# Performance work log

Hardware: AMD Instinct MI355X
Metric: run time of the kernel (lower is better)

Reference implementation:

```python
import jax, jax.numpy as jnp
import numpy as np

NUM_EMBED = 204
HEAD_DIM = 64
B, T = 4, 4096


def setup_inputs() -> dict:
    key = jax.random.key(0)
    kx, kq, kk, kv = jax.random.split(key, 4)
    x = jax.random.normal(kx, (B, T, NUM_EMBED), dtype=jnp.float32)
    s = 1.0 / np.sqrt(NUM_EMBED)
    Wq = jax.random.normal(kq, (NUM_EMBED, HEAD_DIM), dtype=jnp.float32) * s
    Wk = jax.random.normal(kk, (NUM_EMBED, HEAD_DIM), dtype=jnp.float32) * s
    Wv = jax.random.normal(kv, (NUM_EMBED, HEAD_DIM), dtype=jnp.float32) * s
    return {"x": x, "Wq": Wq, "Wk": Wk, "Wv": Wv, "mask": True}


def reference(x, Wq, Wk, Wv, mask):
    # Single-head causal attention. d_k = x.shape[-1] (as in the source, which
    # scales by sqrt of the INPUT embed dim, not head_dim).
    Bn, Tn, d_k = x.shape
    q = x @ Wq  # [B,T,H]
    k = x @ Wk  # [B,T,H]
    v = x @ Wv  # [B,T,H]
    scale = 1.0 / jnp.sqrt(jnp.asarray(d_k, dtype=x.dtype))
    scores = jnp.einsum("bqh,bkh->bqk", q, k) * scale  # [B,T,T]
    if mask:
        causal = jnp.tril(jnp.ones((Tn, Tn), dtype=bool))  # allow j <= i
        scores = jnp.where(causal, scores, jnp.finfo(scores.dtype).min)
    attn = jax.nn.softmax(scores, axis=-1)
    out = jnp.einsum("bqk,bkh->bqh", attn, v)  # [B,T,H]
    # dropout is identity in eval mode
    return out
```

## Files before the change

### kernel.cpp

```cpp
#include <hip/hip_runtime.h>

#define TSEQ   4096
#define NB     4
#define EMB    204
#define HD     64
#define WK     224
#define XSTR   232
#define KSTR   72
#define VSTR   136
#define PSTR   68
#define BIG_NEG (-3.0e38f)

typedef __attribute__((ext_vector_type(8))) short bf16x8;
typedef __attribute__((ext_vector_type(4))) float f32x4;

__device__ __forceinline__ short f2bf(float f) {
    unsigned u = __float_as_uint(f);
    return (short)((u + 0x7fffu + ((u >> 16) & 1u)) >> 16);
}
__device__ __forceinline__ float bf2f(short h) {
    return __uint_as_float(((unsigned)(unsigned short)h) << 16);
}

__global__ __launch_bounds__(256) void prep_zero_kernel(
    const float* __restrict__ Wq,
    const float* __restrict__ Wk,
    const float* __restrict__ Wv,
    short* __restrict__ Wt,
    float* __restrict__ zacc)
{
    int f = blockIdx.x * 256 + threadIdx.x;
    if (f < 3 * HD * WK) {
        int e   = f % WK;
        int h   = (f / WK) % HD;
        int mat = f / (WK * HD);
        const float* W = (mat == 0) ? Wq : (mat == 1) ? Wk : Wv;
        float v = (e < EMB) ? W[e * HD + h] : 0.f;
        Wt[f] = f2bf(v);
    }
    for (int c = blockIdx.x * 256 + threadIdx.x; c < 266240; c += 256 * 256)
        *(float4*)(zacc + c * 4) = make_float4(0.f, 0.f, 0.f, 0.f);
}

__global__ __launch_bounds__(192) void qkv_mfma_kernel(
    const float* __restrict__ x,
    const short* __restrict__ Wt,
    short* __restrict__ qg,
    short* __restrict__ kg,
    short* __restrict__ vtg)
{
    __shared__ __align__(16) short xs[16 * XSTR];

    const int t    = threadIdx.x;
    const int lane = t & 63;
    const int w    = t >> 6;
    const int l15  = lane & 15;
    const int quad = lane >> 4;
    const long long rowb = (long long)blockIdx.x * 16;

    for (int c = t; c < 816; c += 192) {
        int r = c / 51, c4 = c % 51;
        float4 xv = *(const float4*)(x + (rowb + r) * EMB + c4 * 4);
        unsigned p0 = (unsigned)(unsigned short)f2bf(xv.x)
                    | ((unsigned)(unsigned short)f2bf(xv.y) << 16);
        unsigned p1 = (unsigned)(unsigned short)f2bf(xv.z)
                    | ((unsigned)(unsigned short)f2bf(xv.w) << 16);
        uint2 pk; pk.x = p0; pk.y = p1;
        *(uint2*)(&xs[r * XSTR + c4 * 4]) = pk;
    }
    for (int c = t; c < 16 * 28; c += 192) {
        int r = c / 28, cc = c % 28;
        xs[r * XSTR + EMB + cc] = 0;
    }
    __syncthreads();

    f32x4 acc[4];
#pragma unroll
    for (int nt = 0; nt < 4; ++nt) acc[nt] = (f32x4){0.f, 0.f, 0.f, 0.f};

    const short* Wb = Wt + (size_t)w * HD * WK;
#pragma unroll
    for (int ks = 0; ks < 7; ++ks) {
        bf16x8 af = *(const bf16x8*)(&xs[l15 * XSTR + ks * 32 + quad * 8]);
#pragma unroll
        for (int nt = 0; nt < 4; ++nt) {
            bf16x8 bfr = *(const bf16x8*)(Wb + (size_t)(nt * 16 + l15) * WK
                                          + ks * 32 + quad * 8);
            acc[nt] = __builtin_amdgcn_mfma_f32_16x16x32_bf16(af, bfr, acc[nt], 0, 0, 0);
        }
    }

    const float scale = 0.07001400420f;
    if (w == 0) {
#pragma unroll
        for (int r = 0; r < 4; ++r) {
            long long grow = rowb + quad * 4 + r;
#pragma unroll
            for (int nt = 0; nt < 4; ++nt)
                qg[grow * HD + nt * 16 + l15] = f2bf(acc[nt][r] * scale);
        }
    } else if (w == 1) {
#pragma unroll
        for (int r = 0; r < 4; ++r) {
            long long grow = rowb + quad * 4 + r;
#pragma unroll
            for (int nt = 0; nt < 4; ++nt)
                kg[grow * HD + nt * 16 + l15] = f2bf(acc[nt][r]);
        }
    } else {
#pragma unroll
        for (int r = 0; r < 4; ++r) {
            long long grow = rowb + quad * 4 + r;
            int bb = (int)(grow >> 12);
            int tt = (int)(grow & 4095);
#pragma unroll
            for (int nt = 0; nt < 4; ++nt)
                vtg[((long long)bb * HD + nt * 16 + l15) * TSEQ + tt] = f2bf(acc[nt][r]);
        }
    }
}

__global__ __launch_bounds__(256) void flash_mfma_kernel(
    const short* __restrict__ qg,
    const short* __restrict__ kg,
    const short* __restrict__ vtg,
    float* __restrict__ outacc,
    float* __restrict__ lacc)
{
    __shared__ __align__(16) short Ks[128 * KSTR];
    __shared__ __align__(16) short Vt[HD * VSTR];
    __shared__ __align__(16) short Ps[4 * 16 * PSTR];

    const int t    = threadIdx.x;
    const int lane = t & 63;
    const int w    = t >> 6;
    const int pair = w & 1;
    const int par  = w >> 1;
    const int l15  = lane & 15;
    const int quad = lane >> 4;

    const int b = blockIdx.y;
    const int p = 319 - (int)blockIdx.x;

    int a, idx, s;
    if (p < 32)       { a = p >> 2;                idx = p & 3;           s = 1; }
    else if (p < 96)  { a = 8 + ((p - 32) >> 3);   idx = (p - 32) & 7;    s = 2; }
    else if (p < 192) { a = 16 + (p - 96) / 12;    idx = (p - 96) % 12;   s = 3; }
    else              { a = 24 + ((p - 192) >> 4); idx = (p - 192) & 15;  s = 4; }
    const int qt    = 4 * a + idx / s;
    const int split = idx % s;
    const int ntiles = a + 1;
    const int chunk  = (ntiles + s - 1) / s;
    const int kt0    = split * chunk;
    const int kt1    = min(ntiles, kt0 + chunk);

    const int qbase = qt * 32;
    const long long rowb = (long long)b * TSEQ;

    bf16x8 aq[2];
#pragma unroll
    for (int ss = 0; ss < 2; ++ss)
        aq[ss] = *(const bf16x8*)(qg + (rowb + qbase + pair * 16 + l15) * HD
                                  + ss * 32 + quad * 8);

    f32x4 Oacc[4];
#pragma unroll
    for (int nt = 0; nt < 4; ++nt) Oacc[nt] = (f32x4){0.f, 0.f, 0.f, 0.f};
    float lsum[4] = {0.f, 0.f, 0.f, 0.f};

    short* pw = &Ps[w * 16 * PSTR];

    for (int kt = kt0; kt < kt1; ++kt) {
        const int k0 = kt * 128;
        const bool masked = (kt == ntiles - 1);
        __syncthreads();

#pragma unroll
        for (int i = 0; i < 4; ++i) {
            int c = t + i * 256;
            int r = c >> 3, c8 = (c & 7) * 8;
            *(int4*)(&Ks[r * KSTR + c8]) =
                *(const int4*)(kg + (rowb + k0 + r) * HD + c8);
        }
#pragma unroll
        for (int i = 0; i < 4; ++i) {
            int c = t + i * 256;
            int r = c >> 4, c8 = (c & 15) * 8;
            *(int4*)(&Vt[r * VSTR + c8]) =
                *(const int4*)(vtg + ((long long)b * HD + r) * TSEQ + k0 + c8);
        }
        __syncthreads();

        f32x4 S[4];
#pragma unroll
        for (int nt = 0; nt < 4; ++nt) S[nt] = (f32x4){0.f, 0.f, 0.f, 0.f};
#pragma unroll
        for (int ss = 0; ss < 2; ++ss) {
#pragma unroll
            for (int nt = 0; nt < 4; ++nt) {
                bf16x8 bk = *(const bf16x8*)(&Ks[(par * 64 + nt * 16 + l15) * KSTR
                                                 + ss * 32 + quad * 8]);
                S[nt] = __builtin_amdgcn_mfma_f32_16x16x32_bf16(aq[ss], bk, S[nt], 0, 0, 0);
            }
        }

        if (!masked) {
#pragma unroll
            for (int r = 0; r < 4; ++r) {
#pragma unroll
                for (int nt = 0; nt < 4; ++nt) {
                    float pv = __expf(S[nt][r]);
                    short h = f2bf(pv);
                    pw[(quad * 4 + r) * PSTR + nt * 16 + l15] = h;
                    lsum[r] += bf2f(h);
                }
            }
        } else {
#pragma unroll
            for (int r = 0; r < 4; ++r) {
                const int irow = qbase + pair * 16 + quad * 4 + r;
#pragma unroll
                for (int nt = 0; nt < 4; ++nt) {
                    int j = k0 + par * 64 + nt * 16 + l15;
                    float pv = (j <= irow) ? __expf(S[nt][r]) : 0.f;
                    short h = f2bf(pv);
                    pw[(quad * 4 + r) * PSTR + nt * 16 + l15] = h;
                    lsum[r] += bf2f(h);
                }
            }
        }

#pragma unroll
        for (int ss = 0; ss < 2; ++ss) {
            bf16x8 pa = *(const bf16x8*)(&pw[l15 * PSTR + ss * 32 + quad * 8]);
#pragma unroll
            for (int nt = 0; nt < 4; ++nt) {
                bf16x8 vb = *(const bf16x8*)(&Vt[(nt * 16 + l15) * VSTR
                                                 + par * 64 + ss * 32 + quad * 8]);
                Oacc[nt] = __builtin_amdgcn_mfma_f32_16x16x32_bf16(pa, vb, Oacc[nt], 0, 0, 0);
            }
        }
    }

#pragma unroll
    for (int r = 0; r < 4; ++r) {
#pragma unroll
        for (int off = 1; off < 16; off <<= 1)
            lsum[r] += __shfl_xor(lsum[r], off, 64);
    }

    float* oa = outacc + (rowb + qbase + pair * 16) * HD;
#pragma unroll
    for (int r = 0; r < 4; ++r) {
        int row = quad * 4 + r;
#pragma unroll
        for (int nt = 0; nt < 4; ++nt)
            atomicAdd(&oa[row * HD + nt * 16 + l15], Oacc[nt][r]);
        if (l15 == 0)
            atomicAdd(&lacc[rowb + qbase + pair * 16 + row], lsum[r]);
    }
}

__global__ __launch_bounds__(256) void finalize_kernel(
    const float* __restrict__ outacc,
    const float* __restrict__ lacc,
    float* __restrict__ out)
{
    int row = blockIdx.x * 16 + (threadIdx.x >> 4);
    int c4  = (threadIdx.x & 15) * 4;
    float inv = 1.0f / lacc[row];
    float4 v = *(const float4*)(outacc + (size_t)row * HD + c4);
    v.x *= inv; v.y *= inv; v.z *= inv; v.w *= inv;
    *(float4*)(out + (size_t)row * HD + c4) = v;
}

extern "C" void kernel_launch(void* const* d_in, const int* in_sizes, int n_in,
                              void* d_out, int out_size, void* d_ws, size_t ws_size,
                              hipStream_t stream)
{
    const float* x  = (const float*)d_in[0];
    const float* Wq = (const float*)d_in[1];
    const float* Wk = (const float*)d_in[2];
    const float* Wv = (const float*)d_in[3];

    const size_t nrows = (size_t)NB * TSEQ;
    short* qg  = (short*)d_ws;
    short* kg  = qg + nrows * HD;
    short* vtg = kg + nrows * HD;
    short* Wt  = vtg + nrows * HD;
    float* outacc = (float*)(Wt + 3 * HD * WK);
    float* lacc   = outacc + nrows * HD;
    float* outp = (float*)d_out;

    prep_zero_kernel<<<dim3(256), dim3(256), 0, stream>>>(Wq, Wk, Wv, Wt, outacc);
    qkv_mfma_kernel<<<dim3(1024), dim3(192), 0, stream>>>(x, Wt, qg, kg, vtg);
    flash_mfma_kernel<<<dim3(320, NB), dim3(256), 0, stream>>>(qg, kg, vtg, outacc, lacc);
    finalize_kernel<<<dim3(1024), dim3(256), 0, stream>>>(outacc, lacc, outp);
}
```

Measured before the change: 123.8 us.

## Fuse weight prep into QKV kernel, prefetch K/V tiles, compute row sums via MFMA

Merges the weight-transpose and zeroing kernel into the QKV projection kernel. Each block now stages all three bf16 weight matrices in LDS and computes 64 rows of Q, K and V, then writes V^T through an LDS transpose so the global stores are coalesced. In the flash kernel, the next K/V tile is prefetched into registers while the current tile is computed. Softmax row sums are now produced by an MFMA against a ones vector instead of scalar adds and shuffles, and the P stride is padded. The cost is more LDS and registers per block, and each block redundantly reloads and converts the weights.

```diff
diff --git a/kernel.cpp b/kernel.cpp
--- a/kernel.cpp
+++ b/kernel.cpp
@@ -6,9 +6,10 @@
 #define HD     64
 #define WK     224
 #define XSTR   232
+#define WSTR   232
 #define KSTR   72
 #define VSTR   136
-#define PSTR   68
+#define PSTR   72
 #define BIG_NEG (-3.0e38f)
 
 typedef __attribute__((ext_vector_type(8))) short bf16x8;
@@ -18,47 +19,50 @@
     unsigned u = __float_as_uint(f);
     return (short)((u + 0x7fffu + ((u >> 16) & 1u)) >> 16);
 }
-__device__ __forceinline__ float bf2f(short h) {
-    return __uint_as_float(((unsigned)(unsigned short)h) << 16);
-}
-
-__global__ __launch_bounds__(256) void prep_zero_kernel(
+
+__global__ __launch_bounds__(256) void qkv_fused_kernel(
+    const float* __restrict__ x,
     const float* __restrict__ Wq,
     const float* __restrict__ Wk,
     const float* __restrict__ Wv,
-    short* __restrict__ Wt,
-    float* __restrict__ zacc)
-{
-    int f = blockIdx.x * 256 + threadIdx.x;
-    if (f < 3 * HD * WK) {
-        int e   = f % WK;
-        int h   = (f / WK) % HD;
-        int mat = f / (WK * HD);
-        const float* W = (mat == 0) ? Wq : (mat == 1) ? Wk : Wv;
-        float v = (e < EMB) ? W[e * HD + h] : 0.f;
-        Wt[f] = f2bf(v);
-    }
-    for (int c = blockIdx.x * 256 + threadIdx.x; c < 266240; c += 256 * 256)
-        *(float4*)(zacc + c * 4) = make_float4(0.f, 0.f, 0.f, 0.f);
-}
-
-__global__ __launch_bounds__(192) void qkv_mfma_kernel(
-    const float* __restrict__ x,
-    const short* __restrict__ Wt,
     short* __restrict__ qg,
     short* __restrict__ kg,
-    short* __restrict__ vtg)
+    short* __restrict__ vtg,
+    float* __restrict__ outacc,
+    float* __restrict__ lacc)
 {
-    __shared__ __align__(16) short xs[16 * XSTR];
+    __shared__ __align__(16) short xs[64 * XSTR];
+    __shared__ __align__(16) short wl[3 * HD * WSTR];
 
     const int t    = threadIdx.x;
     const int lane = t & 63;
     const int w    = t >> 6;
     const int l15  = lane & 15;
     const int quad = lane >> 4;
-    const long long rowb = (long long)blockIdx.x * 16;
-
-    for (int c = t; c < 816; c += 192) {
+    const long long rowb = (long long)blockIdx.x * 64;
+
+    {
+        float4 z = make_float4(0.f, 0.f, 0.f, 0.f);
+#pragma unroll
+        for (int i = 0; i < 4; ++i)
+            *(float4*)(outacc + rowb * HD + (size_t)(t + i * 256) * 4) = z;
+        if (t < 64) lacc[rowb + t] = 0.f;
+    }
+
+    {
+        const int h = t & 63;
+        const int g = t >> 6;
+#pragma unroll
+        for (int m = 0; m < 3; ++m) {
+            const float* W = (m == 0) ? Wq : (m == 1) ? Wk : Wv;
+            for (int e = g; e < WK; e += 4) {
+                float v = (e < EMB) ? W[e * HD + h] : 0.f;
+                wl[((size_t)m * HD + h) * WSTR + e] = f2bf(v);
+            }
+        }
+    }
+
+    for (int c = t; c < 3264; c += 256) {
         int r = c / 51, c4 = c % 51;
         float4 xv = *(const float4*)(x + (rowb + r) * EMB + c4 * 4);
         unsigned p0 = (unsigned)(unsigned short)f2bf(xv.x)
@@ -68,54 +72,62 @@
         uint2 pk; pk.x = p0; pk.y = p1;
         *(uint2*)(&xs[r * XSTR + c4 * 4]) = pk;
     }
-    for (int c = t; c < 16 * 28; c += 192) {
+    for (int c = t; c < 64 * 28; c += 256) {
         int r = c / 28, cc = c % 28;
         xs[r * XSTR + EMB + cc] = 0;
     }
     __syncthreads();
 
-    f32x4 acc[4];
-#pragma unroll
-    for (int nt = 0; nt < 4; ++nt) acc[nt] = (f32x4){0.f, 0.f, 0.f, 0.f};
-
-    const short* Wb = Wt + (size_t)w * HD * WK;
+    f32x4 acc[3][4];
+#pragma unroll
+    for (int m = 0; m < 3; ++m)
+#pragma unroll
+        for (int nt = 0; nt < 4; ++nt) acc[m][nt] = (f32x4){0.f, 0.f, 0.f, 0.f};
+
 #pragma unroll
     for (int ks = 0; ks < 7; ++ks) {
-        bf16x8 af = *(const bf16x8*)(&xs[l15 * XSTR + ks * 32 + quad * 8]);
+        bf16x8 af = *(const bf16x8*)(&xs[(w * 16 + l15) * XSTR + ks * 32 + quad * 8]);
+#pragma unroll
+        for (int m = 0; m < 3; ++m) {
+#pragma unroll
+            for (int nt = 0; nt < 4; ++nt) {
+                bf16x8 bfr = *(const bf16x8*)(&wl[((size_t)m * HD + nt * 16 + l15) * WSTR
+                                                  + ks * 32 + quad * 8]);
+                acc[m][nt] = __builtin_amdgcn_mfma_f32_16x16x32_bf16(af, bfr, acc[m][nt], 0, 0, 0);
+            }
+        }
+    }
+
+    const float scale = 0.07001400420f;
+#pragma unroll
+    for (int r = 0; r < 4; ++r) {
+        long long grow = rowb + w * 16 + quad * 4 + r;
 #pragma unroll
         for (int nt = 0; nt < 4; ++nt) {
-            bf16x8 bfr = *(const bf16x8*)(Wb + (size_t)(nt * 16 + l15) * WK
-                                          + ks * 32 + quad * 8);
-            acc[nt] = __builtin_amdgcn_mfma_f32_16x16x32_bf16(af, bfr, acc[nt], 0, 0, 0);
-        }
-    }
-
-    const float scale = 0.07001400420f;
-    if (w == 0) {
-#pragma unroll
-        for (int r = 0; r < 4; ++r) {
-            long long grow = rowb + quad * 4 + r;
-#pragma unroll
-            for (int nt = 0; nt < 4; ++nt)
-                qg[grow * HD + nt * 16 + l15] = f2bf(acc[nt][r] * scale);
-        }
-    } else if (w == 1) {
-#pragma unroll
-        for (int r = 0; r < 4; ++r) {
-            long long grow = rowb + quad * 4 + r;
-#pragma unroll
-            for (int nt = 0; nt < 4; ++nt)
-                kg[grow * HD + nt * 16 + l15] = f2bf(acc[nt][r]);
-        }
-    } else {
-#pragma unroll
-        for (int r = 0; r < 4; ++r) {
-            long long grow = rowb + quad * 4 + r;
-            int bb = (int)(grow >> 12);
-            int tt = (int)(grow & 4095);
-#pragma unroll
-            for (int nt = 0; nt < 4; ++nt)
-                vtg[((long long)bb * HD + nt * 16 + l15) * TSEQ + tt] = f2bf(acc[nt][r]);
+            qg[grow * HD + nt * 16 + l15] = f2bf(acc[0][nt][r] * scale);
+            kg[grow * HD + nt * 16 + l15] = f2bf(acc[1][nt][r]);
+        }
+    }
+
+    __syncthreads();
+    short* vts = xs;
+#pragma unroll
+    for (int r = 0; r < 4; ++r) {
+        int tt = w * 16 + quad * 4 + r;
+#pragma unroll
+        for (int nt = 0; nt < 4; ++nt)
+            vts[(nt * 16 + l15) * 72 + tt] = f2bf(acc[2][nt][r]);
+    }
+    __syncthreads();
+    {
+        int bb  = (int)(rowb >> 12);
+        int tt0 = (int)(rowb & 4095);
+#pragma unroll
+        for (int i = 0; i < 2; ++i) {
+            int h = (t >> 3) + i * 32;
+            int c = t & 7;
+            *(int4*)(vtg + ((long long)bb * HD + h) * TSEQ + tt0 + c * 8) =
+                *(const int4*)(&vts[h * 72 + c * 8]);
         }
     }
 }
@@ -147,8 +159,8 @@
     else if (p < 96)  { a = 8 + ((p - 32) >> 3);   idx = (p - 32) & 7;    s = 2; }
     else if (p < 192) { a = 16 + (p - 96) / 12;    idx = (p - 96) % 12;   s = 3; }
     else              { a = 24 + ((p - 192) >> 4); idx = (p - 192) & 15;  s = 4; }
-    const int qt    = 4 * a + idx / s;
-    const int split = idx % s;
+    const int qt     = 4 * a + idx / s;
+    const int split  = idx % s;
     const int ntiles = a + 1;
     const int chunk  = (ntiles + s - 1) / s;
     const int kt0    = split * chunk;
@@ -163,33 +175,55 @@
         aq[ss] = *(const bf16x8*)(qg + (rowb + qbase + pair * 16 + l15) * HD
                                   + ss * 32 + quad * 8);
 
+    bf16x8 ones;
+#pragma unroll
+    for (int j = 0; j < 8; ++j) ones[j] = (short)0x3F80;
+
     f32x4 Oacc[4];
 #pragma unroll
     for (int nt = 0; nt < 4; ++nt) Oacc[nt] = (f32x4){0.f, 0.f, 0.f, 0.f};
-    float lsum[4] = {0.f, 0.f, 0.f, 0.f};
+    f32x4 Lac = (f32x4){0.f, 0.f, 0.f, 0.f};
 
     short* pw = &Ps[w * 16 * PSTR];
 
+    int4 kr[4], vr[4];
+#define LOAD_UNIT(KT)                                                        \
+    {                                                                        \
+        const int _k0 = (KT) * 128;                                          \
+        _Pragma("unroll")                                                    \
+        for (int i = 0; i < 4; ++i) {                                        \
+            int c = t + i * 256;                                             \
+            kr[i] = *(const int4*)(kg + (rowb + _k0 + (c >> 3)) * HD         \
+                                   + (c & 7) * 8);                           \
+        }                                                                    \
+        _Pragma("unroll")                                                    \
+        for (int i = 0; i < 4; ++i) {                                        \
+            int c = t + i * 256;                                             \
+            vr[i] = *(const int4*)(vtg + ((long long)b * HD + (c >> 4)) * TSEQ \
+                                   + _k0 + (c & 15) * 8);                    \
+        }                                                                    \
+    }
+
+    LOAD_UNIT(kt0);
+
     for (int kt = kt0; kt < kt1; ++kt) {
+        const bool masked = (kt == ntiles - 1);
         const int k0 = kt * 128;
-        const bool masked = (kt == ntiles - 1);
         __syncthreads();
 
 #pragma unroll
         for (int i = 0; i < 4; ++i) {
             int c = t + i * 256;
-            int r = c >> 3, c8 = (c & 7) * 8;
-            *(int4*)(&Ks[r * KSTR + c8]) =
-                *(const int4*)(kg + (rowb + k0 + r) * HD + c8);
+            *(int4*)(&Ks[(c >> 3) * KSTR + (c & 7) * 8]) = kr[i];
         }
 #pragma unroll
         for (int i = 0; i < 4; ++i) {
             int c = t + i * 256;
-            int r = c >> 4, c8 = (c & 15) * 8;
-            *(int4*)(&Vt[r * VSTR + c8]) =
-                *(const int4*)(vtg + ((long long)b * HD + r) * TSEQ + k0 + c8);
+            *(int4*)(&Vt[(c >> 4) * VSTR + (c & 15) * 8]) = vr[i];
         }
         __syncthreads();
+
+        if (kt + 1 < kt1) LOAD_UNIT(kt + 1);
 
         f32x4 S[4];
 #pragma unroll
@@ -206,15 +240,10 @@
 
         if (!masked) {
 #pragma unroll
-            for (int r = 0; r < 4; ++r) {
-#pragma unroll
-                for (int nt = 0; nt < 4; ++nt) {
-                    float pv = __expf(S[nt][r]);
-                    short h = f2bf(pv);
-                    pw[(quad * 4 + r) * PSTR + nt * 16 + l15] = h;
-                    lsum[r] += bf2f(h);
-                }
-            }
+            for (int r = 0; r < 4; ++r)
+#pragma unroll
+                for (int nt = 0; nt < 4; ++nt)
+                    pw[(quad * 4 + r) * PSTR + nt * 16 + l15] = f2bf(__expf(S[nt][r]));
         } else {
 #pragma unroll
             for (int r = 0; r < 4; ++r) {
@@ -223,9 +252,7 @@
                 for (int nt = 0; nt < 4; ++nt) {
                     int j = k0 + par * 64 + nt * 16 + l15;
                     float pv = (j <= irow) ? __expf(S[nt][r]) : 0.f;
-                    short h = f2bf(pv);
-                    pw[(quad * 4 + r) * PSTR + nt * 16 + l15] = h;
-                    lsum[r] += bf2f(h);
+                    pw[(quad * 4 + r) * PSTR + nt * 16 + l15] = f2bf(pv);
                 }
             }
         }
@@ -233,6 +260,7 @@
 #pragma unroll
         for (int ss = 0; ss < 2; ++ss) {
             bf16x8 pa = *(const bf16x8*)(&pw[l15 * PSTR + ss * 32 + quad * 8]);
+            Lac = __builtin_amdgcn_mfma_f32_16x16x32_bf16(pa, ones, Lac, 0, 0, 0);
 #pragma unroll
             for (int nt = 0; nt < 4; ++nt) {
                 bf16x8 vb = *(const bf16x8*)(&Vt[(nt * 16 + l15) * VSTR
@@ -241,13 +269,7 @@
             }
         }
     }
-
-#pragma unroll
-    for (int r = 0; r < 4; ++r) {
-#pragma unroll
-        for (int off = 1; off < 16; off <<= 1)
-            lsum[r] += __shfl_xor(lsum[r], off, 64);
-    }
+#undef LOAD_UNIT
 
     float* oa = outacc + (rowb + qbase + pair * 16) * HD;
 #pragma unroll
@@ -257,7 +279,7 @@
         for (int nt = 0; nt < 4; ++nt)
             atomicAdd(&oa[row * HD + nt * 16 + l15], Oacc[nt][r]);
         if (l15 == 0)
-            atomicAdd(&lacc[rowb + qbase + pair * 16 + row], lsum[r]);
+            atomicAdd(&lacc[rowb + qbase + pair * 16 + row], Lac[r]);
     }
 }
 
@@ -287,13 +309,13 @@
     short* qg  = (short*)d_ws;
     short* kg  = qg + nrows * HD;
     short* vtg = kg + nrows * HD;
-    short* Wt  = vtg + nrows * HD;
-    float* outacc = (float*)(Wt + 3 * HD * WK);
+    float* outacc = (float*)(vtg + nrows * HD);
     float* lacc   = outacc + nrows * HD;
     float* outp = (float*)d_out;
 
-    prep_zero_kernel<<<dim3(256), dim3(256), 0, stream>>>(Wq, Wk, Wv, Wt, outacc);
-    qkv_mfma_kernel<<<dim3(1024), dim3(192), 0, stream>>>(x, Wt, qg, kg, vtg);
-    flash_mfma_kernel<<<dim3(320, NB), dim3(256), 0, stream>>>(qg, kg, vtg, outacc, lacc);
+    qkv_fused_kernel<<<dim3(256), dim3(256), 0, stream>>>(
+        x, Wq, Wk, Wv, qg, kg, vtg, outacc, lacc);
+    flash_mfma_kernel<<<dim3(320, NB), dim3(256), 0, stream>>>(
+        qg, kg, vtg, outacc, lacc);
     finalize_kernel<<<dim3(1024), dim3(256), 0, stream>>>(outacc, lacc, outp);
 }
```

Result: slower. 209.7 us (+69.4%).

## Restructure attention as K-block-stationary work units with register-resident K/V

Applied to the files above, without the earlier changes.

Replaces the query-tile flash kernel with a flattened work list of (batch, key block, query 16-row tile) units split evenly across 2048 waves. Each wave keeps a 128-key K and V block in registers, reloading only when the key block changes, and for each query tile computes scores, exp, and the partial output. Every unit then atomically adds its partial output into the accumulator. Row sums come from an MFMA against a ones vector instead of shuffles, and the next Q tile is prefetched. This removes shared-memory K/V staging and block syncs and balances the causal work, at the cost of far more global atomics and heavy register pressure.

```diff
diff --git a/kernel.cpp b/kernel.cpp
--- a/kernel.cpp
+++ b/kernel.cpp
@@ -6,10 +6,7 @@
 #define HD     64
 #define WK     224
 #define XSTR   232
-#define KSTR   72
-#define VSTR   136
-#define PSTR   68
-#define BIG_NEG (-3.0e38f)
+#define PSTR   136
 
 typedef __attribute__((ext_vector_type(8))) short bf16x8;
 typedef __attribute__((ext_vector_type(4))) float f32x4;
@@ -17,9 +14,6 @@
 __device__ __forceinline__ short f2bf(float f) {
     unsigned u = __float_as_uint(f);
     return (short)((u + 0x7fffu + ((u >> 16) & 1u)) >> 16);
-}
-__device__ __forceinline__ float bf2f(short h) {
-    return __uint_as_float(((unsigned)(unsigned short)h) << 16);
 }
 
 __global__ __launch_bounds__(256) void prep_zero_kernel(
@@ -120,144 +114,134 @@
     }
 }
 
-__global__ __launch_bounds__(256) void flash_mfma_kernel(
+__global__ __launch_bounds__(256, 2) void flash_kreg_kernel(
     const short* __restrict__ qg,
     const short* __restrict__ kg,
     const short* __restrict__ vtg,
     float* __restrict__ outacc,
     float* __restrict__ lacc)
 {
-    __shared__ __align__(16) short Ks[128 * KSTR];
-    __shared__ __align__(16) short Vt[HD * VSTR];
     __shared__ __align__(16) short Ps[4 * 16 * PSTR];
 
     const int t    = threadIdx.x;
     const int lane = t & 63;
     const int w    = t >> 6;
-    const int pair = w & 1;
-    const int par  = w >> 1;
     const int l15  = lane & 15;
     const int quad = lane >> 4;
 
-    const int b = blockIdx.y;
-    const int p = 319 - (int)blockIdx.x;
-
-    int a, idx, s;
-    if (p < 32)       { a = p >> 2;                idx = p & 3;           s = 1; }
-    else if (p < 96)  { a = 8 + ((p - 32) >> 3);   idx = (p - 32) & 7;    s = 2; }
-    else if (p < 192) { a = 16 + (p - 96) / 12;    idx = (p - 96) % 12;   s = 3; }
-    else              { a = 24 + ((p - 192) >> 4); idx = (p - 192) & 15;  s = 4; }
-    const int qt    = 4 * a + idx / s;
-    const int split = idx % s;
-    const int ntiles = a + 1;
-    const int chunk  = (ntiles + s - 1) / s;
-    const int kt0    = split * chunk;
-    const int kt1    = min(ntiles, kt0 + chunk);
-
-    const int qbase = qt * 32;
-    const long long rowb = (long long)b * TSEQ;
-
-    bf16x8 aq[2];
-#pragma unroll
-    for (int ss = 0; ss < 2; ++ss)
-        aq[ss] = *(const bf16x8*)(qg + (rowb + qbase + pair * 16 + l15) * HD
-                                  + ss * 32 + quad * 8);
-
-    f32x4 Oacc[4];
-#pragma unroll
-    for (int nt = 0; nt < 4; ++nt) Oacc[nt] = (f32x4){0.f, 0.f, 0.f, 0.f};
-    float lsum[4] = {0.f, 0.f, 0.f, 0.f};
+    const int gw = (int)blockIdx.x * 4 + w;
+    int       u  = (int)(((long long)gw * 16896) >> 11);
+    const int u1 = (int)(((long long)(gw + 1) * 16896) >> 11);
 
     short* pw = &Ps[w * 16 * PSTR];
 
-    for (int kt = kt0; kt < kt1; ++kt) {
-        const int k0 = kt * 128;
-        const bool masked = (kt == ntiles - 1);
-        __syncthreads();
-
-#pragma unroll
-        for (int i = 0; i < 4; ++i) {
-            int c = t + i * 256;
-            int r = c >> 3, c8 = (c & 7) * 8;
-            *(int4*)(&Ks[r * KSTR + c8]) =
-                *(const int4*)(kg + (rowb + k0 + r) * HD + c8);
-        }
-#pragma unroll
-        for (int i = 0; i < 4; ++i) {
-            int c = t + i * 256;
-            int r = c >> 4, c8 = (c & 15) * 8;
-            *(int4*)(&Vt[r * VSTR + c8]) =
-                *(const int4*)(vtg + ((long long)b * HD + r) * TSEQ + k0 + c8);
-        }
-        __syncthreads();
-
-        f32x4 S[4];
-#pragma unroll
-        for (int nt = 0; nt < 4; ++nt) S[nt] = (f32x4){0.f, 0.f, 0.f, 0.f};
-#pragma unroll
-        for (int ss = 0; ss < 2; ++ss) {
-#pragma unroll
-            for (int nt = 0; nt < 4; ++nt) {
-                bf16x8 bk = *(const bf16x8*)(&Ks[(par * 64 + nt * 16 + l15) * KSTR
-                                                 + ss * 32 + quad * 8]);
-                S[nt] = __builtin_amdgcn_mfma_f32_16x16x32_bf16(aq[ss], bk, S[nt], 0, 0, 0);
+    int b  = u / 4224;
+    int r0 = u - b * 4224;
+    int kb = 0;
+    while (r0 >= 256 - 8 * kb) { r0 -= 256 - 8 * kb; ++kb; }
+    int qi = r0;
+
+    bf16x8 ones;
+#pragma unroll
+    for (int j = 0; j < 8; ++j) ones[j] = (short)0x3F80;
+
+    bf16x8 bk[8][2];
+    bf16x8 vb[4][4];
+    long long rowb = (long long)b * TSEQ;
+    int curkb = -1, curb = -1;
+
+    bf16x8 aq[2], aqn[2];
+    {
+        const short* qr = qg + (rowb + kb * 128 + qi * 16 + l15) * HD + quad * 8;
+        aq[0] = *(const bf16x8*)(qr);
+        aq[1] = *(const bf16x8*)(qr + 32);
+    }
+
+    for (; u < u1; ++u) {
+        if (kb != curkb || b != curb) {
+            curkb = kb; curb = b;
+            const int j0r = kb * 128;
+#pragma unroll
+            for (int nt = 0; nt < 8; ++nt) {
+                const short* kr = kg + (rowb + j0r + nt * 16 + l15) * HD + quad * 8;
+                bk[nt][0] = *(const bf16x8*)(kr);
+                bk[nt][1] = *(const bf16x8*)(kr + 32);
             }
+#pragma unroll
+            for (int ss = 0; ss < 4; ++ss)
+#pragma unroll
+                for (int nt = 0; nt < 4; ++nt)
+                    vb[ss][nt] = *(const bf16x8*)(vtg + ((long long)b * HD + nt * 16 + l15) * TSEQ
+                                                  + j0r + ss * 32 + quad * 8);
+        }
+        const int j0 = kb * 128;
+        const int q0 = j0 + qi * 16;
+        const bool masked = (qi < 8);
+
+        f32x4 S[8];
+#pragma unroll
+        for (int nt = 0; nt < 8; ++nt) S[nt] = (f32x4){0.f, 0.f, 0.f, 0.f};
+#pragma unroll
+        for (int ss = 0; ss < 2; ++ss)
+#pragma unroll
+            for (int nt = 0; nt < 8; ++nt)
+                S[nt] = __builtin_amdgcn_mfma_f32_16x16x32_bf16(aq[ss], bk[nt][ss], S[nt], 0, 0, 0);
+
+        int nkb = kb, nqi = qi + 1, nb = b;
+        if (nqi >= 256 - 8 * kb) { nqi = 0; ++nkb; if (nkb >= 32) { nkb = 0; ++nb; } }
+        if (u + 1 < u1) {
+            const short* qr = qg + ((long long)nb * TSEQ + nkb * 128 + nqi * 16 + l15) * HD
+                              + quad * 8;
+            aqn[0] = *(const bf16x8*)(qr);
+            aqn[1] = *(const bf16x8*)(qr + 32);
         }
 
         if (!masked) {
 #pragma unroll
-            for (int r = 0; r < 4; ++r) {
-#pragma unroll
-                for (int nt = 0; nt < 4; ++nt) {
-                    float pv = __expf(S[nt][r]);
-                    short h = f2bf(pv);
-                    pw[(quad * 4 + r) * PSTR + nt * 16 + l15] = h;
-                    lsum[r] += bf2f(h);
+            for (int rr = 0; rr < 4; ++rr)
+#pragma unroll
+                for (int nt = 0; nt < 8; ++nt)
+                    pw[(quad * 4 + rr) * PSTR + nt * 16 + l15] = f2bf(__expf(S[nt][rr]));
+        } else {
+#pragma unroll
+            for (int rr = 0; rr < 4; ++rr) {
+                const int irow = q0 + quad * 4 + rr;
+#pragma unroll
+                for (int nt = 0; nt < 8; ++nt) {
+                    int j = j0 + nt * 16 + l15;
+                    float pv = (j <= irow) ? __expf(S[nt][rr]) : 0.f;
+                    pw[(quad * 4 + rr) * PSTR + nt * 16 + l15] = f2bf(pv);
                 }
             }
-        } else {
-#pragma unroll
-            for (int r = 0; r < 4; ++r) {
-                const int irow = qbase + pair * 16 + quad * 4 + r;
-#pragma unroll
-                for (int nt = 0; nt < 4; ++nt) {
-                    int j = k0 + par * 64 + nt * 16 + l15;
-                    float pv = (j <= irow) ? __expf(S[nt][r]) : 0.f;
-                    short h = f2bf(pv);
-                    pw[(quad * 4 + r) * PSTR + nt * 16 + l15] = h;
-                    lsum[r] += bf2f(h);
-                }
-            }
-        }
-
-#pragma unroll
-        for (int ss = 0; ss < 2; ++ss) {
+        }
+
+        f32x4 O[4];
+#pragma unroll
+        for (int nt = 0; nt < 4; ++nt) O[nt] = (f32x4){0.f, 0.f, 0.f, 0.f};
+        f32x4 L = (f32x4){0.f, 0.f, 0.f, 0.f};
+#pragma unroll
+        for (int ss = 0; ss < 4; ++ss) {
             bf16x8 pa = *(const bf16x8*)(&pw[l15 * PSTR + ss * 32 + quad * 8]);
-#pragma unroll
-            for (int nt = 0; nt < 4; ++nt) {
-                bf16x8 vb = *(const bf16x8*)(&Vt[(nt * 16 + l15) * VSTR
-                                                 + par * 64 + ss * 32 + quad * 8]);
-                Oacc[nt] = __builtin_amdgcn_mfma_f32_16x16x32_bf16(pa, vb, Oacc[nt], 0, 0, 0);
-            }
-        }
-    }
-
-#pragma unroll
-    for (int r = 0; r < 4; ++r) {
-#pragma unroll
-        for (int off = 1; off < 16; off <<= 1)
-            lsum[r] += __shfl_xor(lsum[r], off, 64);
-    }
-
-    float* oa = outacc + (rowb + qbase + pair * 16) * HD;
-#pragma unroll
-    for (int r = 0; r < 4; ++r) {
-        int row = quad * 4 + r;
-#pragma unroll
-        for (int nt = 0; nt < 4; ++nt)
-            atomicAdd(&oa[row * HD + nt * 16 + l15], Oacc[nt][r]);
-        if (l15 == 0)
-            atomicAdd(&lacc[rowb + qbase + pair * 16 + row], lsum[r]);
+            L = __builtin_amdgcn_mfma_f32_16x16x32_bf16(pa, ones, L, 0, 0, 0);
+#pragma unroll
+            for (int nt = 0; nt < 4; ++nt)
+                O[nt] = __builtin_amdgcn_mfma_f32_16x16x32_bf16(pa, vb[ss][nt], O[nt], 0, 0, 0);
+        }
+
+        float* oa = outacc + ((long long)b * TSEQ + q0) * HD;
+#pragma unroll
+        for (int rr = 0; rr < 4; ++rr) {
+            int row = quad * 4 + rr;
+#pragma unroll
+            for (int nt = 0; nt < 4; ++nt)
+                atomicAdd(&oa[row * HD + nt * 16 + l15], O[nt][rr]);
+            if (l15 == 0)
+                atomicAdd(&lacc[(long long)b * TSEQ + q0 + row], L[rr]);
+        }
+
+        aq[0] = aqn[0]; aq[1] = aqn[1];
+        kb = nkb; qi = nqi;
+        if (nb != b) { b = nb; rowb = (long long)b * TSEQ; }
     }
 }
 
@@ -294,6 +278,6 @@
 
     prep_zero_kernel<<<dim3(256), dim3(256), 0, stream>>>(Wq, Wk, Wv, Wt, outacc);
     qkv_mfma_kernel<<<dim3(1024), dim3(192), 0, stream>>>(x, Wt, qg, kg, vtg);
-    flash_mfma_kernel<<<dim3(320, NB), dim3(256), 0, stream>>>(qg, kg, vtg, outacc, lacc);
+    flash_kreg_kernel<<<dim3(512), dim3(256), 0, stream>>>(qg, kg, vtg, outacc, lacc);
     finalize_kernel<<<dim3(1024), dim3(256), 0, stream>>>(outacc, lacc, outp);
 }
```

Result: slower. 158.0 us (+27.7%).

## Compute transposed S=K·Q^T so P stays in registers, row sums via MFMA

Applied to the files above, without the earlier changes.

The attention tile is now computed as K·Q^T, so the exponentiated probabilities come out of the MFMA in the layout needed as the B operand of the P·V MFMA. This removes the per-wave shared-memory round trip for P. Each wave now owns 32 keys instead of a 16-query slice. Row sums are accumulated by an MFMA against a ones vector instead of scalar adds and shuffles. Partial outputs from the four waves are reduced through shared memory, and the result is written directly when the tile is not split (s==1), which avoids atomics there. The P·V MFMA now has half of its K dimension zero-padded, which wastes MFMA throughput. Launch bounds now request 4 blocks per SM.

```diff
diff --git a/kernel.cpp b/kernel.cpp
--- a/kernel.cpp
+++ b/kernel.cpp
@@ -8,18 +8,14 @@
 #define XSTR   232
 #define KSTR   72
 #define VSTR   136
-#define PSTR   68
-#define BIG_NEG (-3.0e38f)
 
 typedef __attribute__((ext_vector_type(8))) short bf16x8;
+typedef __attribute__((ext_vector_type(4))) short s16x4;
 typedef __attribute__((ext_vector_type(4))) float f32x4;
 
 __device__ __forceinline__ short f2bf(float f) {
     unsigned u = __float_as_uint(f);
     return (short)((u + 0x7fffu + ((u >> 16) & 1u)) >> 16);
-}
-__device__ __forceinline__ float bf2f(short h) {
-    return __uint_as_float(((unsigned)(unsigned short)h) << 16);
 }
 
 __global__ __launch_bounds__(256) void prep_zero_kernel(
@@ -120,22 +116,20 @@
     }
 }
 
-__global__ __launch_bounds__(256) void flash_mfma_kernel(
+__global__ __launch_bounds__(256, 4) void flash_mfma_kernel(
     const short* __restrict__ qg,
     const short* __restrict__ kg,
     const short* __restrict__ vtg,
     float* __restrict__ outacc,
     float* __restrict__ lacc)
 {
-    __shared__ __align__(16) short Ks[128 * KSTR];
-    __shared__ __align__(16) short Vt[HD * VSTR];
-    __shared__ __align__(16) short Ps[4 * 16 * PSTR];
+    __shared__ __align__(16) char smem[128 * KSTR * 2 + HD * VSTR * 2];
+    short* Ks = (short*)smem;
+    short* Vt = (short*)(smem + 128 * KSTR * 2);
 
     const int t    = threadIdx.x;
     const int lane = t & 63;
     const int w    = t >> 6;
-    const int pair = w & 1;
-    const int par  = w >> 1;
     const int l15  = lane & 15;
     const int quad = lane >> 4;
 
@@ -147,8 +141,8 @@
     else if (p < 96)  { a = 8 + ((p - 32) >> 3);   idx = (p - 32) & 7;    s = 2; }
     else if (p < 192) { a = 16 + (p - 96) / 12;    idx = (p - 96) % 12;   s = 3; }
     else              { a = 24 + ((p - 192) >> 4); idx = (p - 192) & 15;  s = 4; }
-    const int qt    = 4 * a + idx / s;
-    const int split = idx % s;
+    const int qt     = 4 * a + idx / s;
+    const int split  = idx % s;
     const int ntiles = a + 1;
     const int chunk  = (ntiles + s - 1) / s;
     const int kt0    = split * chunk;
@@ -156,19 +150,28 @@
 
     const int qbase = qt * 32;
     const long long rowb = (long long)b * TSEQ;
-
-    bf16x8 aq[2];
-#pragma unroll
-    for (int ss = 0; ss < 2; ++ss)
-        aq[ss] = *(const bf16x8*)(qg + (rowb + qbase + pair * 16 + l15) * HD
-                                  + ss * 32 + quad * 8);
-
-    f32x4 Oacc[4];
-#pragma unroll
-    for (int nt = 0; nt < 4; ++nt) Oacc[nt] = (f32x4){0.f, 0.f, 0.f, 0.f};
-    float lsum[4] = {0.f, 0.f, 0.f, 0.f};
-
-    short* pw = &Ps[w * 16 * PSTR];
+    const int kwoff = w * 32;
+
+    bf16x8 qfr[2][2];
+#pragma unroll
+    for (int nb = 0; nb < 2; ++nb)
+#pragma unroll
+        for (int ss = 0; ss < 2; ++ss)
+            qfr[nb][ss] = *(const bf16x8*)(qg + (rowb + qbase + nb * 16 + l15) * HD
+                                           + ss * 32 + quad * 8);
+
+    bf16x8 onesA;
+#pragma unroll
+    for (int j = 0; j < 8; ++j) onesA[j] = (j < 4) ? (short)0x3F80 : (short)0;
+
+    f32x4 O[4][2];
+#pragma unroll
+    for (int hm = 0; hm < 4; ++hm)
+#pragma unroll
+        for (int nb = 0; nb < 2; ++nb) O[hm][nb] = (f32x4){0.f, 0.f, 0.f, 0.f};
+    f32x4 L[2];
+    L[0] = (f32x4){0.f, 0.f, 0.f, 0.f};
+    L[1] = (f32x4){0.f, 0.f, 0.f, 0.f};
 
     for (int kt = kt0; kt < kt1; ++kt) {
         const int k0 = kt * 128;
@@ -191,73 +194,92 @@
         }
         __syncthreads();
 
-        f32x4 S[4];
-#pragma unroll
-        for (int nt = 0; nt < 4; ++nt) S[nt] = (f32x4){0.f, 0.f, 0.f, 0.f};
+        f32x4 S[2][2];
+#pragma unroll
+        for (int mb = 0; mb < 2; ++mb)
+#pragma unroll
+            for (int nb = 0; nb < 2; ++nb) S[mb][nb] = (f32x4){0.f, 0.f, 0.f, 0.f};
 #pragma unroll
         for (int ss = 0; ss < 2; ++ss) {
 #pragma unroll
-            for (int nt = 0; nt < 4; ++nt) {
-                bf16x8 bk = *(const bf16x8*)(&Ks[(par * 64 + nt * 16 + l15) * KSTR
+            for (int mb = 0; mb < 2; ++mb) {
+                bf16x8 ka = *(const bf16x8*)(&Ks[(kwoff + mb * 16 + l15) * KSTR
                                                  + ss * 32 + quad * 8]);
-                S[nt] = __builtin_amdgcn_mfma_f32_16x16x32_bf16(aq[ss], bk, S[nt], 0, 0, 0);
+#pragma unroll
+                for (int nb = 0; nb < 2; ++nb)
+                    S[mb][nb] = __builtin_amdgcn_mfma_f32_16x16x32_bf16(ka, qfr[nb][ss],
+                                                                        S[mb][nb], 0, 0, 0);
             }
         }
 
-        if (!masked) {
-#pragma unroll
-            for (int r = 0; r < 4; ++r) {
-#pragma unroll
-                for (int nt = 0; nt < 4; ++nt) {
-                    float pv = __expf(S[nt][r]);
-                    short h = f2bf(pv);
-                    pw[(quad * 4 + r) * PSTR + nt * 16 + l15] = h;
-                    lsum[r] += bf2f(h);
+        bf16x8 pb[2][2];
+#pragma unroll
+        for (int mb = 0; mb < 2; ++mb) {
+#pragma unroll
+            for (int nb = 0; nb < 2; ++nb) {
+                bf16x8 v;
+                if (!masked) {
+#pragma unroll
+                    for (int r = 0; r < 4; ++r) v[r] = f2bf(__expf(S[mb][nb][r]));
+                } else {
+                    const int kkb  = k0 + kwoff + mb * 16 + quad * 4;
+                    const int irow = qbase + nb * 16 + l15;
+#pragma unroll
+                    for (int r = 0; r < 4; ++r) {
+                        float pv = (kkb + r <= irow) ? __expf(S[mb][nb][r]) : 0.f;
+                        v[r] = f2bf(pv);
+                    }
                 }
+#pragma unroll
+                for (int r = 4; r < 8; ++r) v[r] = 0;
+                pb[mb][nb] = v;
+                L[nb] = __builtin_amdgcn_mfma_f32_16x16x32_bf16(onesA, v, L[nb], 0, 0, 0);
             }
-        } else {
-#pragma unroll
-            for (int r = 0; r < 4; ++r) {
-                const int irow = qbase + pair * 16 + quad * 4 + r;
-#pragma unroll
-                for (int nt = 0; nt < 4; ++nt) {
-                    int j = k0 + par * 64 + nt * 16 + l15;
-                    float pv = (j <= irow) ? __expf(S[nt][r]) : 0.f;
-                    short h = f2bf(pv);
-                    pw[(quad * 4 + r) * PSTR + nt * 16 + l15] = h;
-                    lsum[r] += bf2f(h);
-                }
+        }
+
+#pragma unroll
+        for (int mb = 0; mb < 2; ++mb) {
+#pragma unroll
+            for (int hm = 0; hm < 4; ++hm) {
+                s16x4 vv = *(const s16x4*)(&Vt[(hm * 16 + l15) * VSTR
+                                               + kwoff + mb * 16 + quad * 4]);
+                bf16x8 va;
+                va[0] = vv[0]; va[1] = vv[1]; va[2] = vv[2]; va[3] = vv[3];
+                va[4] = 0; va[5] = 0; va[6] = 0; va[7] = 0;
+#pragma unroll
+                for (int nb = 0; nb < 2; ++nb)
+                    O[hm][nb] = __builtin_amdgcn_mfma_f32_16x16x32_bf16(va, pb[mb][nb],
+                                                                        O[hm][nb], 0, 0, 0);
             }
         }
-
-#pragma unroll
-        for (int ss = 0; ss < 2; ++ss) {
-            bf16x8 pa = *(const bf16x8*)(&pw[l15 * PSTR + ss * 32 + quad * 8]);
-#pragma unroll
-            for (int nt = 0; nt < 4; ++nt) {
-                bf16x8 vb = *(const bf16x8*)(&Vt[(nt * 16 + l15) * VSTR
-                                                 + par * 64 + ss * 32 + quad * 8]);
-                Oacc[nt] = __builtin_amdgcn_mfma_f32_16x16x32_bf16(pa, vb, Oacc[nt], 0, 0, 0);
-            }
-        }
-    }
-
-#pragma unroll
-    for (int r = 0; r < 4; ++r) {
-#pragma unroll
-        for (int off = 1; off < 16; off <<= 1)
-            lsum[r] += __shfl_xor(lsum[r], off, 64);
-    }
-
-    float* oa = outacc + (rowb + qbase + pair * 16) * HD;
-#pragma unroll
-    for (int r = 0; r < 4; ++r) {
-        int row = quad * 4 + r;
-#pragma unroll
-        for (int nt = 0; nt < 4; ++nt)
-            atomicAdd(&oa[row * HD + nt * 16 + l15], Oacc[nt][r]);
-        if (l15 == 0)
-            atomicAdd(&lacc[rowb + qbase + pair * 16 + row], lsum[r]);
+    }
+
+    __syncthreads();
+    float* osc = (float*)smem;
+
+    if (quad == 0) {
+#pragma unroll
+        for (int nb = 0; nb < 2; ++nb)
+            atomicAdd(&lacc[rowb + qbase + nb * 16 + l15], L[nb][0]);
+    }
+
+#pragma unroll
+    for (int hm = 0; hm < 4; ++hm)
+#pragma unroll
+        for (int nb = 0; nb < 2; ++nb)
+#pragma unroll
+            for (int r = 0; r < 4; ++r)
+                osc[((w * 64) + hm * 16 + quad * 4 + r) * 33 + nb * 16 + l15] = O[hm][nb][r];
+    __syncthreads();
+
+    float* oa = outacc + (rowb + qbase) * HD;
+#pragma unroll
+    for (int i = 0; i < 8; ++i) {
+        int q = w * 8 + i;
+        float v = osc[(0 * 64 + lane) * 33 + q] + osc[(1 * 64 + lane) * 33 + q]
+                + osc[(2 * 64 + lane) * 33 + q] + osc[(3 * 64 + lane) * 33 + q];
+        if (s == 1) oa[q * HD + lane] = v;
+        else        atomicAdd(&oa[q * HD + lane], v);
     }
 }
 
```

After: 133.2 us. +7.6%, slower.
